# Kernel optimization log

Hardware: AMD Instinct MI355X
Metric: run time of the kernel (lower is better)

Reference implementation:

```python
import jax, jax.numpy as jnp
import numpy as np

LN_EPS = 1e-5

def _gelu(x):
    # matches the module's custom gelu: x * sigmoid(1.702 * x)
    return x * jax.nn.sigmoid(1.702 * x)

def setup_inputs() -> dict:
    key = jax.random.key(0)
    k1, k2, k3, k4 = jax.random.split(key, 4)
    B, d_in, d_out, E = 4096, 768, 1024, 10
    x = jax.random.normal(k1, (B, d_in), dtype=jnp.float32)
    x_cls_logits = jax.random.normal(k2, (B, E), dtype=jnp.float32)
    # expert weights (torch Linear stored transposed; here [in, out] acting as x @ W)
    W1 = jax.random.normal(k3, (E, d_in, d_out), dtype=jnp.float32) * (d_in ** -0.5)
    W2 = jax.random.normal(k4, (E, d_out, d_out), dtype=jnp.float32) * (d_out ** -0.5)
    ln_gamma = jnp.ones((E, d_out), dtype=jnp.float32)
    ln_beta = jnp.zeros((E, d_out), dtype=jnp.float32)
    return {"x": x, "x_cls_logits": x_cls_logits, "W1": W1, "W2": W2,
            "ln_gamma": ln_gamma, "ln_beta": ln_beta}

def reference(x, x_cls_logits, W1, W2, ln_gamma, ln_beta):
    B = x.shape[0]
    # top-1 routing: each sample goes to expert argmax(x_cls)
    cls = jnp.argmax(x_cls_logits, axis=1)                       # [B] int
    # compute all experts densely, then select per sample (grouped equivalent of
    # the per-sample Python-loop dispatch in the original forward)
    embed1_all = jnp.einsum('bi,eio->beo', x, W1)                # [B,E,d_out]
    embed2_all = jnp.einsum('beo,eop->bep', _gelu(embed1_all), W2)  # [B,E,d_out]
    s_all = embed1_all + embed2_all                              # [B,E,d_out]
    rows = jnp.arange(B)
    s = s_all[rows, cls]                                         # [B,d_out]
    # per-expert LayerNorm params gathered per sample
    g = ln_gamma[cls]                                            # [B,d_out]
    b = ln_beta[cls]                                             # [B,d_out]
    mean = jnp.mean(s, axis=-1, keepdims=True)
    var = jnp.mean(jnp.square(s - mean), axis=-1, keepdims=True)
    y = (s - mean) * jax.lax.rsqrt(var + LN_EPS) * g + b
    # L2 normalize embeddings
    out = y / jnp.linalg.norm(y, axis=-1, keepdims=True)
    return out, x_cls_logits
```

## Files before the change

kernel.cpp:

```cpp
#include <hip/hip_runtime.h>
#include <math.h>

#define BSAMP 4096
#define D_IN  768
#define D_OUT 1024
#define NEXP  10
#define LN_EPS 1e-5f
#define STEPS1 (D_IN / 64)
#define STEPS2 (D_OUT / 64)

#define NB_CVT1 (D_IN / 32 * NEXP)
#define NB_CVT2 (D_OUT / 32 * NEXP)
#define NB_XCVT (BSAMP * D_IN / (256 * 16))
#define NB_PREP (1 + NB_CVT1 + NB_CVT2 + NB_XCVT)

typedef __attribute__((ext_vector_type(8))) short bf16x8;
typedef __attribute__((ext_vector_type(4))) float f32x4;

__device__ __forceinline__ float b2f(unsigned short u) {
    union { unsigned int i; float f; } v; v.i = ((unsigned int)u) << 16; return v.f;
}
__device__ __forceinline__ unsigned short f2b(float f) {
    union { float f; unsigned int i; } v; v.f = f;
    unsigned int x = v.i;
    unsigned int r = (x + 0x7fffu + ((x >> 16) & 1u)) >> 16;
    return (unsigned short)r;
}

__device__ __forceinline__ void cvt32(const float* __restrict__ W,
                                      unsigned short* __restrict__ Wt,
                                      int K, int e, int kt, int tid) {
    const int KT = K >> 5;
    const int n  = tid * 4;
    const float* src = W + ((size_t)e * K + (size_t)kt * 32) * D_OUT + n;
    float4 v[32];
    #pragma unroll
    for (int j = 0; j < 32; j++) v[j] = *(const float4*)(src + (size_t)j * D_OUT);
    const int nt = n >> 7, nn = n & 127;
    unsigned short* dst = Wt + ((((size_t)e * 8 + nt) * KT + kt) << 12) + nn * 32;
    #pragma unroll
    for (int c = 0; c < 4; c++) {
        unsigned short t[32];
        #pragma unroll
        for (int j = 0; j < 32; j++) t[j] = f2b(((const float*)&v[j])[c]);
        #pragma unroll
        for (int h = 0; h < 4; h++)
            *(bf16x8*)&dst[c * 32 + h * 8] = *(bf16x8*)&t[h * 8];
    }
}

__global__ __launch_bounds__(256)
void k8_prep(const float* __restrict__ logits, const float* __restrict__ X,
             const float* __restrict__ W1, const float* __restrict__ W2,
             float* __restrict__ out1, int* __restrict__ cls,
             int* __restrict__ idx, int* __restrict__ offs,
             unsigned short* __restrict__ xb, unsigned short* __restrict__ W1t,
             unsigned short* __restrict__ W2t) {
    const int tid = threadIdx.x;
    const int blk = blockIdx.x;

    if (blk == 0) {
        __shared__ int cnt[NEXP];
        __shared__ int cur[NEXP];
        __shared__ int offsL[NEXP + 1];
        if (tid < NEXP) cnt[tid] = 0;
        __syncthreads();

        int be[16];
        #pragma unroll
        for (int j = 0; j < 16; j++) {
            int b = tid + 256 * j;
            const float* L = logits + (size_t)b * NEXP;
            float best = L[0]; int e0 = 0;
            #pragma unroll
            for (int e = 0; e < NEXP; e++) {
                float v = L[e];
                out1[(size_t)b * NEXP + e] = v;
                if (v > best) { best = v; e0 = e; }
            }
            be[j] = e0;
            cls[b] = e0;
            atomicAdd(&cnt[e0], 1);
        }
        __syncthreads();
        if (tid == 0) {
            int s = 0;
            for (int e = 0; e < NEXP; e++) { offsL[e] = s; cur[e] = s; s += cnt[e]; }
            offsL[NEXP] = s;
        }
        __syncthreads();
        if (tid <= NEXP) offs[tid] = offsL[tid];
        #pragma unroll
        for (int j = 0; j < 16; j++) {
            int b = tid + 256 * j;
            int p = atomicAdd(&cur[be[j]], 1);
            idx[p] = b;
        }
        return;
    }

    int i = blk - 1;
    if (i < NB_CVT1) {
        cvt32(W1, W1t, D_IN, i / (D_IN / 32), i % (D_IN / 32), tid);
        return;
    }
    i -= NB_CVT1;
    if (i < NB_CVT2) {
        cvt32(W2, W2t, D_OUT, i / (D_OUT / 32), i % (D_OUT / 32), tid);
        return;
    }
    i -= NB_CVT2;
    {
        int o = (i * 256 + tid) * 16;
        float4 v0 = *(const float4*)(X + o);
        float4 v1 = *(const float4*)(X + o + 4);
        float4 v2 = *(const float4*)(X + o + 8);
        float4 v3 = *(const float4*)(X + o + 12);
        unsigned short t[16] = { f2b(v0.x), f2b(v0.y), f2b(v0.z), f2b(v0.w),
                                 f2b(v1.x), f2b(v1.y), f2b(v1.z), f2b(v1.w),
                                 f2b(v2.x), f2b(v2.y), f2b(v2.z), f2b(v2.w),
                                 f2b(v3.x), f2b(v3.y), f2b(v3.z), f2b(v3.w) };
        *(bf16x8*)(xb + o)     = *(bf16x8*)&t[0];
        *(bf16x8*)(xb + o + 8) = *(bf16x8*)&t[8];
    }
}


#define GLDS(srcp, dstp) __builtin_amdgcn_global_load_lds( \
    (const __attribute__((address_space(1))) unsigned int*)(srcp), \
    (__attribute__((address_space(3))) unsigned int*)(dstp), 16, 0, 0)

#define STAGE_A(Ab, t) do { \
    _Pragma("unroll") \
    for (int j = 0; j < 2; j++) { \
        int c = tid + j * 256; \
        GLDS(aRow + (t) * 64 + (c >> 6) * 8, (Ab) + c * 8); \
    } \
} while (0)

#define STAGE_B(Bb, t) do { \
    _Pragma("unroll") \
    for (int j = 0; j < 4; j++) { \
        int c = tid + j * 256; \
        int kc = c >> 7; \
        GLDS(bPanel + ((size_t)(2 * (t) + (kc >> 2)) << 12) + (c & 127) * 32 + (kc & 3) * 8, \
             (Bb) + c * 8); \
    } \
} while (0)

#define COMPUTE(Ab, Bb) do { \
    _Pragma("unroll") \
    for (int s = 0; s < 2; s++) { \
        const unsigned short* ab_ = (Ab) + (s * 4 + quad) * 512; \
        const unsigned short* bb_ = (Bb) + (s * 4 + quad) * 1024; \
        bf16x8 a0 = *(const bf16x8*)&ab_[(wrow + l16) * 8]; \
        bf16x8 a1 = *(const bf16x8*)&ab_[(wrow + 16 + l16) * 8]; \
        bf16x8 b0 = *(const bf16x8*)&bb_[(wcol + l16) * 8]; \
        bf16x8 b1 = *(const bf16x8*)&bb_[(wcol + 16 + l16) * 8]; \
        bf16x8 b2 = *(const bf16x8*)&bb_[(wcol + 32 + l16) * 8]; \
        bf16x8 b3 = *(const bf16x8*)&bb_[(wcol + 48 + l16) * 8]; \
        acc[0][0] = __builtin_amdgcn_mfma_f32_16x16x32_bf16(a0, b0, acc[0][0], 0, 0, 0); \
        acc[0][1] = __builtin_amdgcn_mfma_f32_16x16x32_bf16(a0, b1, acc[0][1], 0, 0, 0); \
        acc[0][2] = __builtin_amdgcn_mfma_f32_16x16x32_bf16(a0, b2, acc[0][2], 0, 0, 0); \
        acc[0][3] = __builtin_amdgcn_mfma_f32_16x16x32_bf16(a0, b3, acc[0][3], 0, 0, 0); \
        acc[1][0] = __builtin_amdgcn_mfma_f32_16x16x32_bf16(a1, b0, acc[1][0], 0, 0, 0); \
        acc[1][1] = __builtin_amdgcn_mfma_f32_16x16x32_bf16(a1, b1, acc[1][1], 0, 0, 0); \
        acc[1][2] = __builtin_amdgcn_mfma_f32_16x16x32_bf16(a1, b2, acc[1][2], 0, 0, 0); \
        acc[1][3] = __builtin_amdgcn_mfma_f32_16x16x32_bf16(a1, b3, acc[1][3], 0, 0, 0); \
    } \
} while (0)

__global__ __launch_bounds__(256)
void k6_gemm1(const unsigned short* __restrict__ xb, const unsigned short* __restrict__ W1t,
              const int* __restrict__ offs, const int* __restrict__ idx,
              unsigned short* __restrict__ e1g, unsigned short* __restrict__ g1g) {
    const int e = blockIdx.z;
    const int rowStart = offs[e] + blockIdx.y * 64;
    const int rowEnd = offs[e + 1];
    if (rowStart >= rowEnd) return;
    const int nt = blockIdx.x;

    __shared__ __align__(16) unsigned short A0[64 * 64], A1[64 * 64];
    __shared__ __align__(16) unsigned short B0[128 * 64], B1[128 * 64];
    __shared__ int rowIdxL[64];

    const int tid  = threadIdx.x;
    const int lane = tid & 63;
    const int wave = tid >> 6;
    const int quad = lane >> 4;
    const int l16  = lane & 15;
    const int wrow = (wave & 1) * 32;
    const int wcol = (wave >> 1) * 64;

    if (tid < 64) {
        int p = rowStart + tid;
        rowIdxL[tid] = idx[p < rowEnd ? p : rowEnd - 1];
    }
    __syncthreads();

    const unsigned short* aRow   = xb + (size_t)rowIdxL[tid & 63] * D_IN;
    const unsigned short* bPanel = W1t + ((((size_t)e * 8 + nt) * (D_IN / 32)) << 12);

    f32x4 acc[2][4];
    const f32x4 zf = {0.f, 0.f, 0.f, 0.f};
    #pragma unroll
    for (int r = 0; r < 2; r++)
        #pragma unroll
        for (int c = 0; c < 4; c++) acc[r][c] = zf;

    STAGE_A(A0, 0); STAGE_B(B0, 0);
    __syncthreads();
    for (int t = 0; t < STEPS1; t += 2) {
        STAGE_A(A1, t + 1); STAGE_B(B1, t + 1);
        COMPUTE(A0, B0);
        __syncthreads();
        if (t + 2 < STEPS1) { STAGE_A(A0, t + 2); STAGE_B(B0, t + 2); }
        COMPUTE(A1, B1);
        __syncthreads();
    }

    const int n0 = nt * 128;
    #pragma unroll
    for (int r = 0; r < 2; r++)
        #pragma unroll
        for (int q = 0; q < 4; q++) {
            int m = wrow + r * 16 + quad * 4 + q;
            int pp = rowStart + m;
            if (pp < rowEnd) {
                unsigned short* ep = e1g + (size_t)pp * D_OUT + n0 + wcol + l16;
                unsigned short* gp = g1g + (size_t)pp * D_OUT + n0 + wcol + l16;
                #pragma unroll
                for (int c = 0; c < 4; c++) {
                    unsigned short vb = f2b(acc[r][c][q]);
                    ep[c * 16] = vb;
                    float v = b2f(vb);
                    gp[c * 16] = f2b(v / (1.0f + __expf(-1.702f * v)));
                }
            }
        }
}

__global__ __launch_bounds__(256)
void k6_gemm2(const unsigned short* __restrict__ g1g, const unsigned short* __restrict__ e1g,
              const unsigned short* __restrict__ W2t,
              const int* __restrict__ offs, const int* __restrict__ idx,
              float* __restrict__ out0) {
    const int e = blockIdx.z;
    const int rowStart = offs[e] + blockIdx.y * 64;
    const int rowEnd = offs[e + 1];
    if (rowStart >= rowEnd) return;
    const int nt = blockIdx.x;

    __shared__ __align__(16) unsigned short A0[64 * 64], A1[64 * 64];
    __shared__ __align__(16) unsigned short B0[128 * 64], B1[128 * 64];
    __shared__ int rowIdxL[64];

    const int tid  = threadIdx.x;
    const int lane = tid & 63;
    const int wave = tid >> 6;
    const int quad = lane >> 4;
    const int l16  = lane & 15;
    const int wrow = (wave & 1) * 32;
    const int wcol = (wave >> 1) * 64;

    if (tid < 64) {
        int p = rowStart + tid;
        int ps = p < rowEnd ? p : rowEnd - 1;
        rowIdxL[tid] = idx[ps];
    }
    __syncthreads();

    int ap = rowStart + (tid & 63);
    const unsigned short* aRow   = g1g + (size_t)(ap < rowEnd ? ap : rowEnd - 1) * D_OUT;
    const unsigned short* bPanel = W2t + ((((size_t)e * 8 + nt) * (D_OUT / 32)) << 12);

    f32x4 acc[2][4];
    const f32x4 zf = {0.f, 0.f, 0.f, 0.f};
    #pragma unroll
    for (int r = 0; r < 2; r++)
        #pragma unroll
        for (int c = 0; c < 4; c++) acc[r][c] = zf;

    STAGE_A(A0, 0); STAGE_B(B0, 0);
    __syncthreads();
    for (int t = 0; t < STEPS2; t += 2) {
        STAGE_A(A1, t + 1); STAGE_B(B1, t + 1);
        COMPUTE(A0, B0);
        __syncthreads();
        if (t + 2 < STEPS2) { STAGE_A(A0, t + 2); STAGE_B(B0, t + 2); }
        COMPUTE(A1, B1);
        __syncthreads();
    }

    const int n0 = nt * 128;
    #pragma unroll
    for (int r = 0; r < 2; r++)
        #pragma unroll
        for (int q = 0; q < 4; q++) {
            int m = wrow + r * 16 + quad * 4 + q;
            int pp = rowStart + m;
            if (pp < rowEnd) {
                const unsigned short* ep = e1g + (size_t)pp * D_OUT + n0 + wcol + l16;
                float* op = out0 + (size_t)rowIdxL[m] * D_OUT + n0 + wcol + l16;
                #pragma unroll
                for (int c = 0; c < 4; c++)
                    op[c * 16] = acc[r][c][q] + b2f(ep[c * 16]);
            }
        }
}

__global__ __launch_bounds__(256)
void k4_ln(float* __restrict__ out0, const int* __restrict__ cls,
           const float* __restrict__ gam, const float* __restrict__ bet) {
    const int wave = threadIdx.x >> 6;
    const int lane = threadIdx.x & 63;
    const int b = blockIdx.x * 4 + wave;
    const int e = cls[b];

    float* row = out0 + (size_t)b * D_OUT + lane * 16;
    float v[16];
    #pragma unroll
    for (int j = 0; j < 4; j++) {
        float4 t = *(const float4*)(row + j * 4);
        v[j*4] = t.x; v[j*4+1] = t.y; v[j*4+2] = t.z; v[j*4+3] = t.w;
    }

    float sum = 0.f, sq = 0.f;
    #pragma unroll
    for (int j = 0; j < 16; j++) { sum += v[j]; sq += v[j] * v[j]; }
    #pragma unroll
    for (int o = 32; o; o >>= 1) { sum += __shfl_xor(sum, o, 64); sq += __shfl_xor(sq, o, 64); }
    float mean = sum * (1.0f / 1024.0f);
    float var = sq * (1.0f / 1024.0f) - mean * mean;
    float inv = rsqrtf(var + LN_EPS);

    const float* gp = gam + (size_t)e * D_OUT + lane * 16;
    const float* bp = bet + (size_t)e * D_OUT + lane * 16;
    float y[16]; float y2 = 0.f;
    #pragma unroll
    for (int j = 0; j < 16; j++) {
        y[j] = (v[j] - mean) * inv * gp[j] + bp[j];
        y2 += y[j] * y[j];
    }
    #pragma unroll
    for (int o = 32; o; o >>= 1) y2 += __shfl_xor(y2, o, 64);
    float rn = rsqrtf(y2);

    #pragma unroll
    for (int j = 0; j < 4; j++) {
        float4 t = { y[j*4] * rn, y[j*4+1] * rn, y[j*4+2] * rn, y[j*4+3] * rn };
        *(float4*)(row + j * 4) = t;
    }
}

extern "C" void kernel_launch(void* const* d_in, const int* in_sizes, int n_in,
                              void* d_out, int out_size, void* d_ws, size_t ws_size,
                              hipStream_t stream) {
    const float* x   = (const float*)d_in[0];
    const float* lg  = (const float*)d_in[1];
    const float* W1  = (const float*)d_in[2];
    const float* W2  = (const float*)d_in[3];
    const float* gam = (const float*)d_in[4];
    const float* bet = (const float*)d_in[5];
    float* out0 = (float*)d_out;
    float* out1 = out0 + (size_t)BSAMP * D_OUT;

    char* ws = (char*)d_ws;
    int* offs = (int*)ws;
    int* cls  = offs + 16;
    int* idx  = cls + BSAMP;
    unsigned short* W1t = (unsigned short*)(ws + 65536);
    unsigned short* W2t = W1t + (size_t)NEXP * D_IN * D_OUT;
    unsigned short* e1g = W2t + (size_t)NEXP * D_OUT * D_OUT;
    unsigned short* g1g = e1g + (size_t)BSAMP * D_OUT;
    unsigned short* xb  = g1g + (size_t)BSAMP * D_OUT;

    k8_prep<<<NB_PREP, 256, 0, stream>>>(lg, x, W1, W2, out1, cls, idx, offs,
                                         xb, W1t, W2t);

    dim3 g1(8, 64, NEXP);
    k6_gemm1<<<g1, 256, 0, stream>>>(xb, W1t, offs, idx, e1g, g1g);

    dim3 g2(8, 64, NEXP);
    k6_gemm2<<<g2, 256, 0, stream>>>(g1g, e1g, W2t, offs, idx, out0);

    k4_ln<<<BSAMP / 4, 256, 0, stream>>>(out0, cls, gam, bet);
}
```

Measured before the change: 215.9 us.

## Fuse LayerNorm into GEMM2 via last-block ticket and make routing deterministic

Removes the separate LayerNorm kernel. Each GEMM2 block atomically increments a per-(expert,row-tile) counter, and the last of the 8 column-tile blocks runs LayerNorm plus L2 normalisation over that tile's rows. It also replaces the shared-memory atomic scatter in routing with per-thread counts and prefix sums, giving a deterministic index order. This saves a kernel launch and its separate pass, at the cost of threadfences, atomics and a serial tail of work on the last block of each tile.

After: 352.0 us. 63.0% more time.

```diff
diff --git a/kernel.cpp b/kernel.cpp
--- a/kernel.cpp
+++ b/kernel.cpp
@@ -53,20 +53,19 @@
 void k8_prep(const float* __restrict__ logits, const float* __restrict__ X,
              const float* __restrict__ W1, const float* __restrict__ W2,
              float* __restrict__ out1, int* __restrict__ cls,
-             int* __restrict__ idx, int* __restrict__ offs,
+             int* __restrict__ idx, int* __restrict__ offs, int* __restrict__ rtcnt,
              unsigned short* __restrict__ xb, unsigned short* __restrict__ W1t,
              unsigned short* __restrict__ W2t) {
     const int tid = threadIdx.x;
     const int blk = blockIdx.x;
 
     if (blk == 0) {
-        __shared__ int cnt[NEXP];
-        __shared__ int cur[NEXP];
-        __shared__ int offsL[NEXP + 1];
-        if (tid < NEXP) cnt[tid] = 0;
-        __syncthreads();
-
+        __shared__ int scnt[NEXP][256];
+        __shared__ int ebase[NEXP + 1];
         int be[16];
+        int lcnt[NEXP];
+        #pragma unroll
+        for (int e = 0; e < NEXP; e++) lcnt[e] = 0;
         #pragma unroll
         for (int j = 0; j < 16; j++) {
             int b = tid + 256 * j;
@@ -80,21 +79,32 @@
             }
             be[j] = e0;
             cls[b] = e0;
-            atomicAdd(&cnt[e0], 1);
+            #pragma unroll
+            for (int e = 0; e < NEXP; e++) lcnt[e] += (e0 == e) ? 1 : 0;
+        }
+        #pragma unroll
+        for (int e = 0; e < NEXP; e++) scnt[e][tid] = lcnt[e];
+        for (int r = tid; r < NEXP * 64; r += 256) rtcnt[r] = 0;
+        __syncthreads();
+        if (tid < NEXP) {
+            int s = 0;
+            for (int i = 0; i < 256; i++) { int c = scnt[tid][i]; scnt[tid][i] = s; s += c; }
+            ebase[tid + 1] = s;
         }
         __syncthreads();
         if (tid == 0) {
-            int s = 0;
-            for (int e = 0; e < NEXP; e++) { offsL[e] = s; cur[e] = s; s += cnt[e]; }
-            offsL[NEXP] = s;
-        }
-        __syncthreads();
-        if (tid <= NEXP) offs[tid] = offsL[tid];
-        #pragma unroll
-        for (int j = 0; j < 16; j++) {
-            int b = tid + 256 * j;
-            int p = atomicAdd(&cur[be[j]], 1);
-            idx[p] = b;
+            ebase[0] = 0;
+            for (int e = 0; e < NEXP; e++) ebase[e + 1] += ebase[e];
+        }
+        __syncthreads();
+        if (tid <= NEXP) offs[tid] = ebase[tid];
+        #pragma unroll
+        for (int e = 0; e < NEXP; e++) {
+            int pos = ebase[e] + scnt[e][tid];
+            #pragma unroll
+            for (int j = 0; j < 16; j++) {
+                if (be[j] == e) idx[pos++] = tid + 256 * j;
+            }
         }
         return;
     }
@@ -241,10 +251,11 @@
 }
 
 __global__ __launch_bounds__(256)
-void k6_gemm2(const unsigned short* __restrict__ g1g, const unsigned short* __restrict__ e1g,
-              const unsigned short* __restrict__ W2t,
-              const int* __restrict__ offs, const int* __restrict__ idx,
-              float* __restrict__ out0) {
+void k9_gemm2ln(const unsigned short* __restrict__ g1g, const unsigned short* __restrict__ e1g,
+                const unsigned short* __restrict__ W2t,
+                const int* __restrict__ offs, const int* __restrict__ idx,
+                const float* __restrict__ gam, const float* __restrict__ bet,
+                int* __restrict__ rtcnt, float* __restrict__ out0) {
     const int e = blockIdx.z;
     const int rowStart = offs[e] + blockIdx.y * 64;
     const int rowEnd = offs[e + 1];
@@ -254,6 +265,7 @@
     __shared__ __align__(16) unsigned short A0[64 * 64], A1[64 * 64];
     __shared__ __align__(16) unsigned short B0[128 * 64], B1[128 * 64];
     __shared__ int rowIdxL[64];
+    __shared__ int ticket;
 
     const int tid  = threadIdx.x;
     const int lane = tid & 63;
@@ -307,49 +319,56 @@
                     op[c * 16] = acc[r][c][q] + b2f(ep[c * 16]);
             }
         }
-}
-
-__global__ __launch_bounds__(256)
-void k4_ln(float* __restrict__ out0, const int* __restrict__ cls,
-           const float* __restrict__ gam, const float* __restrict__ bet) {
-    const int wave = threadIdx.x >> 6;
-    const int lane = threadIdx.x & 63;
-    const int b = blockIdx.x * 4 + wave;
-    const int e = cls[b];
-
-    float* row = out0 + (size_t)b * D_OUT + lane * 16;
-    float v[16];
+
+    __threadfence();
+    __syncthreads();
+    if (tid == 0) ticket = atomicAdd(&rtcnt[e * 64 + blockIdx.y], 1);
+    __syncthreads();
+    if (ticket != 7) return;
+    __threadfence();
+
+    const float* gpt = gam + (size_t)e * D_OUT + lane * 16;
+    const float* bpt = bet + (size_t)e * D_OUT + lane * 16;
+    float gv[16], bv[16];
     #pragma unroll
     for (int j = 0; j < 4; j++) {
-        float4 t = *(const float4*)(row + j * 4);
-        v[j*4] = t.x; v[j*4+1] = t.y; v[j*4+2] = t.z; v[j*4+3] = t.w;
-    }
-
-    float sum = 0.f, sq = 0.f;
-    #pragma unroll
-    for (int j = 0; j < 16; j++) { sum += v[j]; sq += v[j] * v[j]; }
-    #pragma unroll
-    for (int o = 32; o; o >>= 1) { sum += __shfl_xor(sum, o, 64); sq += __shfl_xor(sq, o, 64); }
-    float mean = sum * (1.0f / 1024.0f);
-    float var = sq * (1.0f / 1024.0f) - mean * mean;
-    float inv = rsqrtf(var + LN_EPS);
-
-    const float* gp = gam + (size_t)e * D_OUT + lane * 16;
-    const float* bp = bet + (size_t)e * D_OUT + lane * 16;
-    float y[16]; float y2 = 0.f;
-    #pragma unroll
-    for (int j = 0; j < 16; j++) {
-        y[j] = (v[j] - mean) * inv * gp[j] + bp[j];
-        y2 += y[j] * y[j];
-    }
-    #pragma unroll
-    for (int o = 32; o; o >>= 1) y2 += __shfl_xor(y2, o, 64);
-    float rn = rsqrtf(y2);
-
-    #pragma unroll
-    for (int j = 0; j < 4; j++) {
-        float4 t = { y[j*4] * rn, y[j*4+1] * rn, y[j*4+2] * rn, y[j*4+3] * rn };
-        *(float4*)(row + j * 4) = t;
+        float4 tg = *(const float4*)(gpt + j * 4);
+        gv[j*4] = tg.x; gv[j*4+1] = tg.y; gv[j*4+2] = tg.z; gv[j*4+3] = tg.w;
+        float4 tb = *(const float4*)(bpt + j * 4);
+        bv[j*4] = tb.x; bv[j*4+1] = tb.y; bv[j*4+2] = tb.z; bv[j*4+3] = tb.w;
+    }
+
+    const int nrows = (rowEnd - rowStart) < 64 ? (rowEnd - rowStart) : 64;
+    for (int m = wave; m < nrows; m += 4) {
+        float* row = out0 + (size_t)rowIdxL[m] * D_OUT + lane * 16;
+        float v[16];
+        #pragma unroll
+        for (int j = 0; j < 4; j++) {
+            float4 t = *(const float4*)(row + j * 4);
+            v[j*4] = t.x; v[j*4+1] = t.y; v[j*4+2] = t.z; v[j*4+3] = t.w;
+        }
+        float sum = 0.f, sq = 0.f;
+        #pragma unroll
+        for (int j = 0; j < 16; j++) { sum += v[j]; sq += v[j] * v[j]; }
+        #pragma unroll
+        for (int o = 32; o; o >>= 1) { sum += __shfl_xor(sum, o, 64); sq += __shfl_xor(sq, o, 64); }
+        float mean = sum * (1.0f / 1024.0f);
+        float var = sq * (1.0f / 1024.0f) - mean * mean;
+        float inv = rsqrtf(var + LN_EPS);
+        float y[16]; float y2 = 0.f;
+        #pragma unroll
+        for (int j = 0; j < 16; j++) {
+            y[j] = (v[j] - mean) * inv * gv[j] + bv[j];
+            y2 += y[j] * y[j];
+        }
+        #pragma unroll
+        for (int o = 32; o; o >>= 1) y2 += __shfl_xor(y2, o, 64);
+        float rn = rsqrtf(y2);
+        #pragma unroll
+        for (int j = 0; j < 4; j++) {
+            float4 t = { y[j*4] * rn, y[j*4+1] * rn, y[j*4+2] * rn, y[j*4+3] * rn };
+            *(float4*)(row + j * 4) = t;
+        }
     }
 }
 
@@ -366,23 +385,22 @@
     float* out1 = out0 + (size_t)BSAMP * D_OUT;
 
     char* ws = (char*)d_ws;
-    int* offs = (int*)ws;
-    int* cls  = offs + 16;
-    int* idx  = cls + BSAMP;
+    int* offs  = (int*)ws;
+    int* cls   = offs + 16;
+    int* idx   = cls + BSAMP;
+    int* rtcnt = idx + BSAMP;
     unsigned short* W1t = (unsigned short*)(ws + 65536);
     unsigned short* W2t = W1t + (size_t)NEXP * D_IN * D_OUT;
     unsigned short* e1g = W2t + (size_t)NEXP * D_OUT * D_OUT;
     unsigned short* g1g = e1g + (size_t)BSAMP * D_OUT;
     unsigned short* xb  = g1g + (size_t)BSAMP * D_OUT;
 
-    k8_prep<<<NB_PREP, 256, 0, stream>>>(lg, x, W1, W2, out1, cls, idx, offs,
+    k8_prep<<<NB_PREP, 256, 0, stream>>>(lg, x, W1, W2, out1, cls, idx, offs, rtcnt,
                                          xb, W1t, W2t);
 
     dim3 g1(8, 64, NEXP);
     k6_gemm1<<<g1, 256, 0, stream>>>(xb, W1t, offs, idx, e1g, g1g);
 
     dim3 g2(8, 64, NEXP);
-    k6_gemm2<<<g2, 256, 0, stream>>>(g1g, e1g, W2t, offs, idx, out0);
-
-    k4_ln<<<BSAMP / 4, 256, 0, stream>>>(out0, cls, gam, bet);
-}
+    k9_gemm2ln<<<g2, 256, 0, stream>>>(g1g, e1g, W2t, offs, idx, gam, bet, rtcnt, out0);
+}
```
